# Optimization experiments

Measured on AMD Instinct MI355X. Metric: run time of the kernel, lower is better.

## Reference

```python
import math
import jax, jax.numpy as jnp
import numpy as np

B, N, D, E, DN, H, M = 32, 64, 256, 32, 64, 8, 32
EPS = 1e-5


def _ln(x):
    # param-free layer norm over the last axis
    mu = jnp.mean(x, axis=-1, keepdims=True)
    var = jnp.var(x, axis=-1, keepdims=True)
    return (x - mu) * jax.lax.rsqrt(var + EPS)


def setup_inputs() -> dict:
    key = jax.random.key(0)
    ks = jax.random.split(key, 9)
    embeddings = jax.random.normal(ks[0], (B, N, D), dtype=jnp.float32)
    edge_features = jax.random.normal(ks[1], (B, N, N, E), dtype=jnp.float32)
    mask = jax.random.randint(ks[2], (B, N), 0, 2).astype(bool)
    node_features = jax.random.normal(ks[3], (B, N, DN), dtype=jnp.float32)
    s = lambda d: 1.0 / math.sqrt(d)
    W_edge = jax.random.normal(ks[4], (E, H, M), dtype=jnp.float32) * s(E)
    W_recv = jax.random.normal(ks[5], (D, H, M), dtype=jnp.float32) * s(D)
    W_send = jax.random.normal(ks[6], (D, H, M), dtype=jnp.float32) * s(D)
    W_recv_node = jax.random.normal(ks[7], (DN, H, M), dtype=jnp.float32) * s(DN)
    W_send_node = jax.random.normal(ks[8], (DN, H, M), dtype=jnp.float32) * s(DN)
    return dict(embeddings=embeddings, edge_features=edge_features, mask=mask,
                node_features=node_features, W_edge=W_edge, W_recv=W_recv,
                W_send=W_send, W_recv_node=W_recv_node, W_send_node=W_send_node)


def reference(embeddings, edge_features, mask, node_features,
              W_edge, W_recv, W_send, W_recv_node, W_send_node):
    sqrt2 = math.sqrt(2.0)
    mask_f = mask.astype(embeddings.dtype)  # [B, N]
    emb = _ln(embeddings) * mask_f[..., None]  # [B, N, D]
    # double mask: [B, sender, receiver, 1]
    dm = (mask_f[..., None, :, None] * mask_f[..., :, None, None])
    ef = edge_features * dm  # [B, N, N, E]
    # projections to (heads, message_dim)
    edge_part = jnp.einsum('bije,ehm->bijhm', ef, W_edge)        # [B,N,N,H,M]
    recv = jnp.einsum('bjd,dhm->bjhm', emb, W_recv) / sqrt2      # [B,N,H,M]
    send = jnp.einsum('bid,dhm->bihm', emb, W_send) / sqrt2
    # receiver broadcast over sender axis (-4), sender over receiver axis (-3)
    rs = jnp.tanh(recv[..., None, :, :, :] + send[..., :, None, :, :])  # [B,N,N,H,M]
    rn = jnp.einsum('bjd,dhm->bjhm', node_features, W_recv_node)
    sn = jnp.einsum('bid,dhm->bihm', node_features, W_send_node)
    rs = rs * jax.nn.sigmoid((rn[..., None, :, :, :] + sn[..., :, None, :, :]) / sqrt2)
    msgs = rs * edge_part * dm[..., None]  # [B,N,N,H,M]
    updates = msgs.sum(axis=-4)            # sum over senders -> [B,N,H,M]
    updates = _ln(updates)
    return jnp.reshape(updates, (*updates.shape[:-2], -1))  # [B,N,H*M]
```

## Files before the change

### kernel.cpp

```cpp
#include <hip/hip_runtime.h>
#include <hip/hip_bf16.h>
#include <math.h>

#define B_   32
#define N_   64
#define D_   256
#define E_   32
#define DN_  64
#define H_   8
#define M_   32
#define HM_  256
#define BN_  2048
#define EPS_ 1e-5f
#define SQRT2_    1.41421356237309515f
#define NINVSQ2_ (-0.70710678118654752f)

typedef float f32x4 __attribute__((ext_vector_type(4)));
typedef short bf16x8 __attribute__((ext_vector_type(8)));
union U4S8 { uint4 u; bf16x8 s; };

__device__ __forceinline__ unsigned pk2(float a, float b) {
    union { __hip_bfloat162 h; unsigned u; } cv;
    cv.h = __float22bfloat162_rn(make_float2(a, b));
    return cv.u;
}


__device__ __forceinline__ void remap(int wg, int& b, int& s) {
    const int xcd = wg & 7;
    b = xcd * 4 + (wg >> 7);
    s = (wg >> 3) & 15;
}

__device__ __forceinline__ unsigned long long mask_bits(
        const int* mraw, int b, int t, int w, int l, int* s_flag_sh,
        unsigned long long* bits_sh) {
    if (t == 0) *s_flag_sh = 0;
    __syncthreads();
    { int v0 = mraw[t], v1 = mraw[t + 256];
      if (((v0 | v1) & ~1) != 0) atomicOr(s_flag_sh, 1); }
    __syncthreads();
    const bool bytef = (*s_flag_sh != 0);
    const unsigned char* mbb = (const unsigned char*)mraw;
    if (w == 0) {
        const int k = b * N_ + l;
        const bool on = bytef ? (mbb[k] != 0) : (mraw[k] != 0);
        unsigned long long bits = __ballot(on);
        if (l == 0) *bits_sh = bits;
    }
    __syncthreads();
    return *bits_sh;
}

__global__ __launch_bounds__(256, 4) void node_k(
        const float* __restrict__ emb, const float* __restrict__ nfeat,
        const int* __restrict__ mraw,
        const float* __restrict__ Wr, const float* __restrict__ Ws,
        const float* __restrict__ Wrn, const float* __restrict__ Wsn,
        float2* __restrict__ g_rr, float2* __restrict__ g_ssC) {
    const int t = threadIdx.x;
    const int w = t >> 6, l = t & 63, hi = l >> 4, lo = l & 15;
    int b, s; remap(blockIdx.x, b, s);

    __shared__ int s_flag;
    __shared__ unsigned long long bits_sh;
    const unsigned long long bits = mask_bits(mraw, b, t, w, l, &s_flag, &bits_sh);
    const int cb = __popcll(bits);

    float mu_l, rs_l;
    {
        const int qrow = w * 16 + (l >> 2);
        const float* rp = emb + (size_t)(b * N_ + qrow) * D_ + (l & 3) * 64;
        float sv = 0.f, s2 = 0.f;
        #pragma unroll
        for (int k = 0; k < 16; ++k) {
            float4 x = *(const float4*)(rp + k * 4);
            sv += x.x + x.y + x.z + x.w;
            s2 += x.x*x.x + x.y*x.y + x.z*x.z + x.w*x.w;
        }
        sv += __shfl_xor(sv, 1); sv += __shfl_xor(sv, 2);
        s2 += __shfl_xor(s2, 1); s2 += __shfl_xor(s2, 2);
        float mu  = sv * (1.0f / D_);
        float var = s2 * (1.0f / D_) - mu * mu;
        float rs  = rsqrtf(var + EPS_) * (((bits >> qrow) & 1ull) ? 1.0f : 0.0f);
        mu_l = __shfl(mu, lo << 2);
        rs_l = __shfl(rs, lo << 2);
    }

    const int nb = s * 16 + lo;
    const float* arow = emb   + (size_t)(b * N_ + w * 16 + lo) * D_  + hi * 8;
    const float* nrow = nfeat + (size_t)(b * N_ + w * 16 + lo) * DN_ + hi * 8;
    f32x4 aR = {0,0,0,0}, aS = {0,0,0,0}, aRN = {0,0,0,0}, aSN = {0,0,0,0};
    #pragma unroll
    for (int ks = 0; ks < 8; ++ks) {
        float4 xa = *(const float4*)(arow + ks * 32);
        float4 xb = *(const float4*)(arow + ks * 32 + 4);
        U4S8 a;
        a.u = make_uint4(pk2((xa.x - mu_l) * rs_l, (xa.y - mu_l) * rs_l),
                         pk2((xa.z - mu_l) * rs_l, (xa.w - mu_l) * rs_l),
                         pk2((xb.x - mu_l) * rs_l, (xb.y - mu_l) * rs_l),
                         pk2((xb.z - mu_l) * rs_l, (xb.w - mu_l) * rs_l));
        const float* wrp = Wr + (size_t)(ks * 32 + hi * 8) * HM_ + nb;
        const float* wsp = Ws + (size_t)(ks * 32 + hi * 8) * HM_ + nb;
        U4S8 br, bs;
        br.u = make_uint4(pk2(wrp[0],     wrp[HM_]),    pk2(wrp[2*HM_], wrp[3*HM_]),
                          pk2(wrp[4*HM_], wrp[5*HM_]),  pk2(wrp[6*HM_], wrp[7*HM_]));
        bs.u = make_uint4(pk2(wsp[0],     wsp[HM_]),    pk2(wsp[2*HM_], wsp[3*HM_]),
                          pk2(wsp[4*HM_], wsp[5*HM_]),  pk2(wsp[6*HM_], wsp[7*HM_]));
        aR = __builtin_amdgcn_mfma_f32_16x16x32_bf16(a.s, br.s, aR, 0, 0, 0);
        aS = __builtin_amdgcn_mfma_f32_16x16x32_bf16(a.s, bs.s, aS, 0, 0, 0);
        if (ks < 2) {
            float4 na = *(const float4*)(nrow + ks * 32);
            float4 nb4 = *(const float4*)(nrow + ks * 32 + 4);
            U4S8 a2;
            a2.u = make_uint4(pk2(na.x, na.y),  pk2(na.z, na.w),
                              pk2(nb4.x, nb4.y), pk2(nb4.z, nb4.w));
            const float* wrn = Wrn + (size_t)(ks * 32 + hi * 8) * HM_ + nb;
            const float* wsn = Wsn + (size_t)(ks * 32 + hi * 8) * HM_ + nb;
            U4S8 brn, bsn;
            brn.u = make_uint4(pk2(wrn[0],     wrn[HM_]),   pk2(wrn[2*HM_], wrn[3*HM_]),
                               pk2(wrn[4*HM_], wrn[5*HM_]), pk2(wrn[6*HM_], wrn[7*HM_]));
            bsn.u = make_uint4(pk2(wsn[0],     wsn[HM_]),   pk2(wsn[2*HM_], wsn[3*HM_]),
                               pk2(wsn[4*HM_], wsn[5*HM_]), pk2(wsn[6*HM_], wsn[7*HM_]));
            aRN = __builtin_amdgcn_mfma_f32_16x16x32_bf16(a2.s, brn.s, aRN, 0, 0, 0);
            aSN = __builtin_amdgcn_mfma_f32_16x16x32_bf16(a2.s, bsn.s, aSN, 0, 0, 0);
        }
    }

    #pragma unroll
    for (int r = 0; r < 4; ++r) {
        const int i = w * 16 + hi * 4 + r;
        g_rr[(size_t)(b * N_ + i) * HM_ + nb] =
            make_float2(__expf(SQRT2_ * aR[r]), __expf(NINVSQ2_ * aRN[r]));
        if ((bits >> i) & 1ull) {
            const int p = __popcll(bits & ((1ull << i) - 1ull));
            g_ssC[(size_t)(b * N_ + p) * HM_ + nb] =
                make_float2(__expf(SQRT2_ * aS[r]), __expf(NINVSQ2_ * aSN[r]));
        }
    }
    for (int p = cb + (t >> 4); p < N_; p += 16)
        g_ssC[(size_t)(b * N_ + p) * HM_ + s * 16 + (t & 15)] = make_float2(0.f, 0.f);
}

__global__ __launch_bounds__(256, 4) void edge_k(
        const float* __restrict__ edge, const float* __restrict__ We,
        const int* __restrict__ mraw,
        const float2* __restrict__ g_rr, const float2* __restrict__ g_ssC,
        float* __restrict__ out) {
    const int t = threadIdx.x;
    const int w = t >> 6, l = t & 63, hi = l >> 4, lo = l & 15;
    int b, s; remap(blockIdx.x, b, s);
    const int j0 = s * 4;

    __shared__ int s_flag;
    __shared__ unsigned long long bits_sh;
    __shared__ int sidx_s[N_];
    __shared__ __align__(16) uint4 ldsA[4][256];

    const unsigned long long bits = mask_bits(mraw, b, t, w, l, &s_flag, &bits_sh);
    const int cb = __popcll(bits);
    if (w == 0) {
        const bool on = (bits >> l) & 1ull;
        int p = __popcll(bits & ((1ull << l) - 1ull));
        if (on) sidx_s[p] = l;
        if (l >= cb) sidx_s[l] = -1;
    }
    __syncthreads();

    if (((bits >> j0) & 15ull) == 0ull) {
        #pragma unroll
        for (int q = 0; q < 4; ++q)
            out[(size_t)(b * N_ + j0 + q) * HM_ + t] = 0.0f;
        return;
    }

    {
        const int mt = t >> 6, phi = (t >> 4) & 3, plo = t & 15;
        const int si = sidx_s[mt * 16 + plo];
        if (si >= 0) {
            const float* rb = edge + ((size_t)((b * N_ + si) * N_ + j0)) * E_ + phi * 8;
            #pragma unroll
            for (int q = 0; q < 4; ++q) {
                float4 v0 = *(const float4*)(rb + q * E_);
                float4 v1 = *(const float4*)(rb + q * E_ + 4);
                ldsA[q][t] = make_uint4(pk2(v0.x, v0.y), pk2(v0.z, v0.w),
                                        pk2(v1.x, v1.y), pk2(v1.z, v1.w));
            }
        } else {
            #pragma unroll
            for (int q = 0; q < 4; ++q) ldsA[q][t] = make_uint4(0, 0, 0, 0);
        }
    }
    __syncthreads();

    U4S8 b4[4];
    #pragma unroll
    for (int nl = 0; nl < 4; ++nl) {
        const float* wp = We + (size_t)(hi * 8) * HM_ + w * 64 + nl * 16 + lo;
        b4[nl].u = make_uint4(pk2(wp[0],     wp[HM_]),    pk2(wp[2*HM_], wp[3*HM_]),
                              pk2(wp[4*HM_], wp[5*HM_]),  pk2(wp[6*HM_], wp[7*HM_]));
    }

    float2 rrq[4][4];
    #pragma unroll
    for (int q = 0; q < 4; ++q)
        #pragma unroll
        for (int nl = 0; nl < 4; ++nl)
            rrq[q][nl] = g_rr[(size_t)(b * N_ + j0 + q) * HM_ + w * 64 + nl * 16 + lo];

    float upd[4][4];
    #pragma unroll
    for (int q = 0; q < 4; ++q)
        #pragma unroll
        for (int nl = 0; nl < 4; ++nl) upd[q][nl] = 0.0f;

    const f32x4 zero = {0.0f, 0.0f, 0.0f, 0.0f};
    #pragma unroll
    for (int mt = 0; mt < 4; ++mt) {
        if (mt * 16 < cb) {
            float2 ssv[4][4];
            #pragma unroll
            for (int r = 0; r < 4; ++r) {
                const float2* srow =
                    g_ssC + (size_t)(b * N_ + mt * 16 + hi * 4 + r) * HM_ + w * 64 + lo;
                #pragma unroll
                for (int nl = 0; nl < 4; ++nl) ssv[r][nl] = srow[nl * 16];
            }
            #pragma unroll
            for (int q = 0; q < 4; ++q) {
                if ((bits >> (j0 + q)) & 1ull) {
                    U4S8 a; a.u = ldsA[q][mt * 64 + l];
                    f32x4 acc[4];
                    #pragma unroll
                    for (int nl = 0; nl < 4; ++nl)
                        acc[nl] = __builtin_amdgcn_mfma_f32_16x16x32_bf16(a.s, b4[nl].s, zero, 0, 0, 0);
                    #pragma unroll
                    for (int r = 0; r < 4; ++r)
                        #pragma unroll
                        for (int nl = 0; nl < 4; ++nl) {
                            float u = rrq[q][nl].x * ssv[r][nl].x;
                            float v = rrq[q][nl].y * ssv[r][nl].y;
                            float den = (u + 1.0f) * (v + 1.0f);
                            float g = (u - 1.0f) * __builtin_amdgcn_rcpf(den);
                            upd[q][nl] = fmaf(g, acc[nl][r], upd[q][nl]);
                        }
                }
            }
        }
    }
    #pragma unroll
    for (int q = 0; q < 4; ++q) {
        const int j = j0 + q, bn = b * N_ + j;
        if (!((bits >> j) & 1ull)) {
            out[(size_t)bn * HM_ + w * 64 + l] = 0.0f;
            continue;
        }
        float u0 = upd[q][0], u1 = upd[q][1], u2 = upd[q][2], u3 = upd[q][3];
        u0 += __shfl_xor(u0, 16); u0 += __shfl_xor(u0, 32);
        u1 += __shfl_xor(u1, 16); u1 += __shfl_xor(u1, 32);
        u2 += __shfl_xor(u2, 16); u2 += __shfl_xor(u2, 32);
        u3 += __shfl_xor(u3, 16); u3 += __shfl_xor(u3, 32);
        float s0 = u0 + u1, q0 = u0*u0 + u1*u1;
        float s1 = u2 + u3, q1 = u2*u2 + u3*u3;
        #pragma unroll
        for (int k = 8; k >= 1; k >>= 1) {
            s0 += __shfl_xor(s0, k); q0 += __shfl_xor(q0, k);
            s1 += __shfl_xor(s1, k); q1 += __shfl_xor(q1, k);
        }
        float mu0 = s0 * (1.0f / M_), va0 = q0 * (1.0f / M_) - mu0 * mu0;
        float mu1 = s1 * (1.0f / M_), va1 = q1 * (1.0f / M_) - mu1 * mu1;
        float rs0 = rsqrtf(va0 + EPS_), rs1 = rsqrtf(va1 + EPS_);
        float v01 = (hi & 1) ? u1 : u0;
        float v23 = (hi & 1) ? u3 : u2;
        float val = (hi < 2) ? v01 : v23;
        float o = (hi < 2) ? (val - mu0) * rs0 : (val - mu1) * rs1;
        out[(size_t)bn * HM_ + w * 64 + l] = o;
    }
}

extern "C" void kernel_launch(void* const* d_in, const int* in_sizes, int n_in,
                              void* d_out, int out_size, void* d_ws, size_t ws_size,
                              hipStream_t stream) {
    const float* embeddings = (const float*)d_in[0];
    const float* edge_feat  = (const float*)d_in[1];
    const int*   mask_raw   = (const int*)d_in[2];
    const float* node_feat  = (const float*)d_in[3];
    const float* W_edge     = (const float*)d_in[4];
    const float* W_recv     = (const float*)d_in[5];
    const float* W_send     = (const float*)d_in[6];
    const float* W_recvn    = (const float*)d_in[7];
    const float* W_sendn    = (const float*)d_in[8];
    float* out = (float*)d_out;

    float2* g_ssC = (float2*)d_ws;
    float2* g_rr  = g_ssC + (size_t)BN_ * HM_;

    node_k<<<512, 256, 0, stream>>>(embeddings, node_feat, mask_raw,
                                    W_recv, W_send, W_recvn, W_sendn,
                                    g_rr, g_ssC);
    edge_k<<<512, 256, 0, stream>>>(edge_feat, W_edge, mask_raw,
                                    g_rr, g_ssC, out);
}
```

Baseline: 41.27 us.

## Split node projection across send/recv waves and halve receivers per edge block

The node kernel now launches 512-thread blocks where waves 0-3 compute the receiver projections and waves 4-7 compute the sender projections, so each wave does half the MFMA work. The edge kernel processes 2 receivers per block instead of 4 and launches 1024 blocks, with the MFMAs hoisted ahead of the gating loop. The aim is more parallelism and shorter per-wave dependency chains. The cost is reloading the sender gate values (g_ssC) and edge weights per block twice as often, and dropping the per-receiver mask skip inside the loop.

```diff
diff --git a/kernel.cpp b/kernel.cpp
--- a/kernel.cpp
+++ b/kernel.cpp
@@ -26,10 +26,13 @@
 }
 
 
-__device__ __forceinline__ void remap(int wg, int& b, int& s) {
-    const int xcd = wg & 7;
-    b = xcd * 4 + (wg >> 7);
+__device__ __forceinline__ void remap512(int wg, int& b, int& s) {
+    b = (wg & 7) * 4 + (wg >> 7);
     s = (wg >> 3) & 15;
+}
+__device__ __forceinline__ void remap1024(int wg, int& b, int& s) {
+    b = (wg & 7) * 4 + (wg >> 8);
+    s = (wg >> 3) & 31;
 }
 
 __device__ __forceinline__ unsigned long long mask_bits(
@@ -37,7 +40,8 @@
         unsigned long long* bits_sh) {
     if (t == 0) *s_flag_sh = 0;
     __syncthreads();
-    { int v0 = mraw[t], v1 = mraw[t + 256];
+    { const int ti = t & 255;
+      int v0 = mraw[ti], v1 = mraw[ti + 256];
       if (((v0 | v1) & ~1) != 0) atomicOr(s_flag_sh, 1); }
     __syncthreads();
     const bool bytef = (*s_flag_sh != 0);
@@ -52,7 +56,7 @@
     return *bits_sh;
 }
 
-__global__ __launch_bounds__(256, 4) void node_k(
+__global__ __launch_bounds__(512, 4) void node_k(
         const float* __restrict__ emb, const float* __restrict__ nfeat,
         const int* __restrict__ mraw,
         const float* __restrict__ Wr, const float* __restrict__ Ws,
@@ -60,7 +64,9 @@
         float2* __restrict__ g_rr, float2* __restrict__ g_ssC) {
     const int t = threadIdx.x;
     const int w = t >> 6, l = t & 63, hi = l >> 4, lo = l & 15;
-    int b, s; remap(blockIdx.x, b, s);
+    const int rt = w & 3;
+    const int sendside = w >> 2;
+    int b, s; remap512(blockIdx.x, b, s);
 
     __shared__ int s_flag;
     __shared__ unsigned long long bits_sh;
@@ -69,7 +75,7 @@
 
     float mu_l, rs_l;
     {
-        const int qrow = w * 16 + (l >> 2);
+        const int qrow = rt * 16 + (l >> 2);
         const float* rp = emb + (size_t)(b * N_ + qrow) * D_ + (l & 3) * 64;
         float sv = 0.f, s2 = 0.f;
         #pragma unroll
@@ -87,10 +93,12 @@
         rs_l = __shfl(rs, lo << 2);
     }
 
+    const float* W1 = sendside ? Ws  : Wr;
+    const float* W2 = sendside ? Wsn : Wrn;
     const int nb = s * 16 + lo;
-    const float* arow = emb   + (size_t)(b * N_ + w * 16 + lo) * D_  + hi * 8;
-    const float* nrow = nfeat + (size_t)(b * N_ + w * 16 + lo) * DN_ + hi * 8;
-    f32x4 aR = {0,0,0,0}, aS = {0,0,0,0}, aRN = {0,0,0,0}, aSN = {0,0,0,0};
+    const float* arow = emb   + (size_t)(b * N_ + rt * 16 + lo) * D_  + hi * 8;
+    const float* nrow = nfeat + (size_t)(b * N_ + rt * 16 + lo) * DN_ + hi * 8;
+    f32x4 a1 = {0,0,0,0}, a2 = {0,0,0,0};
     #pragma unroll
     for (int ks = 0; ks < 8; ++ks) {
         float4 xa = *(const float4*)(arow + ks * 32);
@@ -100,46 +108,41 @@
                          pk2((xa.z - mu_l) * rs_l, (xa.w - mu_l) * rs_l),
                          pk2((xb.x - mu_l) * rs_l, (xb.y - mu_l) * rs_l),
                          pk2((xb.z - mu_l) * rs_l, (xb.w - mu_l) * rs_l));
-        const float* wrp = Wr + (size_t)(ks * 32 + hi * 8) * HM_ + nb;
-        const float* wsp = Ws + (size_t)(ks * 32 + hi * 8) * HM_ + nb;
-        U4S8 br, bs;
-        br.u = make_uint4(pk2(wrp[0],     wrp[HM_]),    pk2(wrp[2*HM_], wrp[3*HM_]),
-                          pk2(wrp[4*HM_], wrp[5*HM_]),  pk2(wrp[6*HM_], wrp[7*HM_]));
-        bs.u = make_uint4(pk2(wsp[0],     wsp[HM_]),    pk2(wsp[2*HM_], wsp[3*HM_]),
-                          pk2(wsp[4*HM_], wsp[5*HM_]),  pk2(wsp[6*HM_], wsp[7*HM_]));
-        aR = __builtin_amdgcn_mfma_f32_16x16x32_bf16(a.s, br.s, aR, 0, 0, 0);
-        aS = __builtin_amdgcn_mfma_f32_16x16x32_bf16(a.s, bs.s, aS, 0, 0, 0);
+        const float* wp = W1 + (size_t)(ks * 32 + hi * 8) * HM_ + nb;
+        U4S8 bfr;
+        bfr.u = make_uint4(pk2(wp[0],     wp[HM_]),    pk2(wp[2*HM_], wp[3*HM_]),
+                           pk2(wp[4*HM_], wp[5*HM_]),  pk2(wp[6*HM_], wp[7*HM_]));
+        a1 = __builtin_amdgcn_mfma_f32_16x16x32_bf16(a.s, bfr.s, a1, 0, 0, 0);
         if (ks < 2) {
-            float4 na = *(const float4*)(nrow + ks * 32);
+            float4 na  = *(const float4*)(nrow + ks * 32);
             float4 nb4 = *(const float4*)(nrow + ks * 32 + 4);
-            U4S8 a2;
-            a2.u = make_uint4(pk2(na.x, na.y),  pk2(na.z, na.w),
+            U4S8 an;
+            an.u = make_uint4(pk2(na.x, na.y),   pk2(na.z, na.w),
                               pk2(nb4.x, nb4.y), pk2(nb4.z, nb4.w));
-            const float* wrn = Wrn + (size_t)(ks * 32 + hi * 8) * HM_ + nb;
-            const float* wsn = Wsn + (size_t)(ks * 32 + hi * 8) * HM_ + nb;
-            U4S8 brn, bsn;
-            brn.u = make_uint4(pk2(wrn[0],     wrn[HM_]),   pk2(wrn[2*HM_], wrn[3*HM_]),
-                               pk2(wrn[4*HM_], wrn[5*HM_]), pk2(wrn[6*HM_], wrn[7*HM_]));
-            bsn.u = make_uint4(pk2(wsn[0],     wsn[HM_]),   pk2(wsn[2*HM_], wsn[3*HM_]),
-                               pk2(wsn[4*HM_], wsn[5*HM_]), pk2(wsn[6*HM_], wsn[7*HM_]));
-            aRN = __builtin_amdgcn_mfma_f32_16x16x32_bf16(a2.s, brn.s, aRN, 0, 0, 0);
-            aSN = __builtin_amdgcn_mfma_f32_16x16x32_bf16(a2.s, bsn.s, aSN, 0, 0, 0);
+            const float* wn = W2 + (size_t)(ks * 32 + hi * 8) * HM_ + nb;
+            U4S8 bn;
+            bn.u = make_uint4(pk2(wn[0],     wn[HM_]),    pk2(wn[2*HM_], wn[3*HM_]),
+                              pk2(wn[4*HM_], wn[5*HM_]),  pk2(wn[6*HM_], wn[7*HM_]));
+            a2 = __builtin_amdgcn_mfma_f32_16x16x32_bf16(an.s, bn.s, a2, 0, 0, 0);
         }
     }
 
     #pragma unroll
     for (int r = 0; r < 4; ++r) {
-        const int i = w * 16 + hi * 4 + r;
-        g_rr[(size_t)(b * N_ + i) * HM_ + nb] =
-            make_float2(__expf(SQRT2_ * aR[r]), __expf(NINVSQ2_ * aRN[r]));
-        if ((bits >> i) & 1ull) {
+        const int i = rt * 16 + hi * 4 + r;
+        float2 v = make_float2(__expf(SQRT2_ * a1[r]), __expf(NINVSQ2_ * a2[r]));
+        if (sendside == 0) {
+            g_rr[(size_t)(b * N_ + i) * HM_ + nb] = v;
+        } else if ((bits >> i) & 1ull) {
             const int p = __popcll(bits & ((1ull << i) - 1ull));
-            g_ssC[(size_t)(b * N_ + p) * HM_ + nb] =
-                make_float2(__expf(SQRT2_ * aS[r]), __expf(NINVSQ2_ * aSN[r]));
-        }
-    }
-    for (int p = cb + (t >> 4); p < N_; p += 16)
-        g_ssC[(size_t)(b * N_ + p) * HM_ + s * 16 + (t & 15)] = make_float2(0.f, 0.f);
+            g_ssC[(size_t)(b * N_ + p) * HM_ + nb] = v;
+        }
+    }
+    if (sendside) {
+        const int tt = t - 256;
+        for (int p = cb + (tt >> 4); p < N_; p += 16)
+            g_ssC[(size_t)(b * N_ + p) * HM_ + s * 16 + (tt & 15)] = make_float2(0.f, 0.f);
+    }
 }
 
 __global__ __launch_bounds__(256, 4) void edge_k(
@@ -149,13 +152,13 @@
         float* __restrict__ out) {
     const int t = threadIdx.x;
     const int w = t >> 6, l = t & 63, hi = l >> 4, lo = l & 15;
-    int b, s; remap(blockIdx.x, b, s);
-    const int j0 = s * 4;
+    int b, s; remap1024(blockIdx.x, b, s);
+    const int j0 = s * 2;
 
     __shared__ int s_flag;
     __shared__ unsigned long long bits_sh;
     __shared__ int sidx_s[N_];
-    __shared__ __align__(16) uint4 ldsA[4][256];
+    __shared__ __align__(16) uint4 ldsA[2][256];
 
     const unsigned long long bits = mask_bits(mraw, b, t, w, l, &s_flag, &bits_sh);
     const int cb = __popcll(bits);
@@ -167,9 +170,9 @@
     }
     __syncthreads();
 
-    if (((bits >> j0) & 15ull) == 0ull) {
-        #pragma unroll
-        for (int q = 0; q < 4; ++q)
+    if (((bits >> j0) & 3ull) == 0ull) {
+        #pragma unroll
+        for (int q = 0; q < 2; ++q)
             out[(size_t)(b * N_ + j0 + q) * HM_ + t] = 0.0f;
         return;
     }
@@ -180,7 +183,7 @@
         if (si >= 0) {
             const float* rb = edge + ((size_t)((b * N_ + si) * N_ + j0)) * E_ + phi * 8;
             #pragma unroll
-            for (int q = 0; q < 4; ++q) {
+            for (int q = 0; q < 2; ++q) {
                 float4 v0 = *(const float4*)(rb + q * E_);
                 float4 v1 = *(const float4*)(rb + q * E_ + 4);
                 ldsA[q][t] = make_uint4(pk2(v0.x, v0.y), pk2(v0.z, v0.w),
@@ -188,7 +191,7 @@
             }
         } else {
             #pragma unroll
-            for (int q = 0; q < 4; ++q) ldsA[q][t] = make_uint4(0, 0, 0, 0);
+            for (int q = 0; q < 2; ++q) ldsA[q][t] = make_uint4(0, 0, 0, 0);
         }
     }
     __syncthreads();
@@ -201,16 +204,16 @@
                               pk2(wp[4*HM_], wp[5*HM_]),  pk2(wp[6*HM_], wp[7*HM_]));
     }
 
-    float2 rrq[4][4];
-    #pragma unroll
-    for (int q = 0; q < 4; ++q)
+    float2 rrq[2][4];
+    #pragma unroll
+    for (int q = 0; q < 2; ++q)
         #pragma unroll
         for (int nl = 0; nl < 4; ++nl)
             rrq[q][nl] = g_rr[(size_t)(b * N_ + j0 + q) * HM_ + w * 64 + nl * 16 + lo];
 
-    float upd[4][4];
-    #pragma unroll
-    for (int q = 0; q < 4; ++q)
+    float upd[2][4];
+    #pragma unroll
+    for (int q = 0; q < 2; ++q)
         #pragma unroll
         for (int nl = 0; nl < 4; ++nl) upd[q][nl] = 0.0f;
 
@@ -218,38 +221,36 @@
     #pragma unroll
     for (int mt = 0; mt < 4; ++mt) {
         if (mt * 16 < cb) {
-            float2 ssv[4][4];
+            f32x4 acc[2][4];
+            #pragma unroll
+            for (int q = 0; q < 2; ++q) {
+                U4S8 a; a.u = ldsA[q][mt * 64 + l];
+                #pragma unroll
+                for (int nl = 0; nl < 4; ++nl)
+                    acc[q][nl] = __builtin_amdgcn_mfma_f32_16x16x32_bf16(a.s, b4[nl].s, zero, 0, 0, 0);
+            }
             #pragma unroll
             for (int r = 0; r < 4; ++r) {
                 const float2* srow =
                     g_ssC + (size_t)(b * N_ + mt * 16 + hi * 4 + r) * HM_ + w * 64 + lo;
+                float2 ssv[4];
                 #pragma unroll
-                for (int nl = 0; nl < 4; ++nl) ssv[r][nl] = srow[nl * 16];
+                for (int nl = 0; nl < 4; ++nl) ssv[nl] = srow[nl * 16];
+                #pragma unroll
+                for (int q = 0; q < 2; ++q)
+                    #pragma unroll
+                    for (int nl = 0; nl < 4; ++nl) {
+                        float u = rrq[q][nl].x * ssv[nl].x;
+                        float v = rrq[q][nl].y * ssv[nl].y;
+                        float den = (u + 1.0f) * (v + 1.0f);
+                        float g = (u - 1.0f) * __builtin_amdgcn_rcpf(den);
+                        upd[q][nl] = fmaf(g, acc[q][nl][r], upd[q][nl]);
+                    }
             }
-            #pragma unroll
-            for (int q = 0; q < 4; ++q) {
-                if ((bits >> (j0 + q)) & 1ull) {
-                    U4S8 a; a.u = ldsA[q][mt * 64 + l];
-                    f32x4 acc[4];
-                    #pragma unroll
-                    for (int nl = 0; nl < 4; ++nl)
-                        acc[nl] = __builtin_amdgcn_mfma_f32_16x16x32_bf16(a.s, b4[nl].s, zero, 0, 0, 0);
-                    #pragma unroll
-                    for (int r = 0; r < 4; ++r)
-                        #pragma unroll
-                        for (int nl = 0; nl < 4; ++nl) {
-                            float u = rrq[q][nl].x * ssv[r][nl].x;
-                            float v = rrq[q][nl].y * ssv[r][nl].y;
-                            float den = (u + 1.0f) * (v + 1.0f);
-                            float g = (u - 1.0f) * __builtin_amdgcn_rcpf(den);
-                            upd[q][nl] = fmaf(g, acc[nl][r], upd[q][nl]);
-                        }
-                }
-            }
-        }
-    }
-    #pragma unroll
-    for (int q = 0; q < 4; ++q) {
+        }
+    }
+    #pragma unroll
+    for (int q = 0; q < 2; ++q) {
         const int j = j0 + q, bn = b * N_ + j;
         if (!((bits >> j) & 1ull)) {
             out[(size_t)bn * HM_ + w * 64 + l] = 0.0f;
@@ -295,9 +296,9 @@
     float2* g_ssC = (float2*)d_ws;
     float2* g_rr  = g_ssC + (size_t)BN_ * HM_;
 
-    node_k<<<512, 256, 0, stream>>>(embeddings, node_feat, mask_raw,
+    node_k<<<512, 512, 0, stream>>>(embeddings, node_feat, mask_raw,
                                     W_recv, W_send, W_recvn, W_sendn,
                                     g_rr, g_ssC);
-    edge_k<<<512, 256, 0, stream>>>(edge_feat, W_edge, mask_raw,
-                                    g_rr, g_ssC, out);
-}
+    edge_k<<<1024, 256, 0, stream>>>(edge_feat, W_edge, mask_raw,
+                                     g_rr, g_ssC, out);
+}
```

Measured after the change: 39.06 us. 5.3% less time.
